# Performance work log

Measured on AMD Instinct MI355X. Metric: run time of the kernel, lower is better.

## Reference

```python
import jax, jax.numpy as jnp
import numpy as np

BIN_SIZE = 256
TOP_K = 16


def setup_inputs() -> dict:
    key = jax.random.key(0)
    kx, kc = jax.random.split(key)
    x = jax.random.normal(kx, (2, 4096, 512), dtype=jnp.float32)
    codebook = jax.random.normal(kc, (512, 16), dtype=jnp.float32)  # (feature_dim, max_num_bins//2)
    return {"x": x, "codebook": codebook}


def reference(x, codebook):
    B, N, F = x.shape
    n_bins = N // BIN_SIZE  # 16
    # LSH bucket assignment: project onto random hyperplanes, pick argmax of [p, -p]
    mul = x @ codebook[:, : n_bins // 2]                      # (B, N, n_bins//2)
    cmul = jnp.concatenate([mul, -mul], axis=-1)              # (B, N, n_bins)
    bin_idx = jnp.argmax(cmul, axis=-1)                       # (B, N)
    # argsort-based binning: equal-size bins of points sorted by bucket id
    bins_split = jnp.argsort(bin_idx, axis=-1).reshape(B, n_bins, BIN_SIZE)
    # gather points into bins: (B, n_bins, bin_size, F)
    points_binned = jnp.take_along_axis(x[:, None, :, :], bins_split[..., None], axis=2)
    # intra-bin dense similarity + sigmoid
    dm = jax.nn.sigmoid(jnp.einsum('bnif,bnjf->bnij', points_binned, points_binned))
    vals, idx = jax.lax.top_k(dm, TOP_K)                      # (B, n_bins, bin_size, k)
    # map local bin indices back to global point indices
    dst = jnp.take_along_axis(bins_split[:, :, None, :], idx, axis=-1)  # (B, nb, bs, k)
    src = jnp.broadcast_to(bins_split[..., None], dst.shape)
    b = jnp.broadcast_to(jnp.arange(B)[:, None, None, None], dst.shape)
    # dense equivalent of the coalesced batched sparse_coo_tensor of size (N, N)
    out = jnp.zeros((B, N, N), dtype=x.dtype).at[b, src, dst].add(vals)
    return out
```

## Files before the change

kernel.cpp:

```cpp
#include <hip/hip_runtime.h>
#include <stdint.h>
#include <math.h>

#define NPTS 4096
#define NF 512
#define NBINS 16
#define BSZ 256
#define TOPK 16
#define NBATCH 2
#define SHALF (NBATCH * NBINS * BSZ * BSZ)

__global__ __launch_bounds__(256) void k_assign(const float* __restrict__ x,
                                                const float* __restrict__ cb,
                                                int* __restrict__ bin_idx) {
    int gw   = (blockIdx.x * 256 + threadIdx.x) >> 6;
    int lane = threadIdx.x & 63;
    const float* row = x + (size_t)gw * NF;
    float acc[8];
#pragma unroll
    for (int j = 0; j < 8; j++) acc[j] = 0.f;
    for (int f = lane; f < NF; f += 64) {
        float xv = row[f];
        const float4* c = (const float4*)(cb + f * 16);
        float4 c0 = c[0], c1 = c[1];
        acc[0] += xv * c0.x; acc[1] += xv * c0.y; acc[2] += xv * c0.z; acc[3] += xv * c0.w;
        acc[4] += xv * c1.x; acc[5] += xv * c1.y; acc[6] += xv * c1.z; acc[7] += xv * c1.w;
    }
#pragma unroll
    for (int off = 32; off > 0; off >>= 1) {
#pragma unroll
        for (int j = 0; j < 8; j++) acc[j] += __shfl_xor(acc[j], off, 64);
    }
    if (lane == 0) {
        float best = acc[0]; int bi = 0;
#pragma unroll
        for (int j = 1; j < 8; j++) { if (acc[j] > best) { best = acc[j]; bi = j; } }
#pragma unroll
        for (int j = 0; j < 8; j++) { float v = -acc[j]; if (v > best) { best = v; bi = 8 + j; } }
        bin_idx[gw] = bi;
    }
}

__global__ __launch_bounds__(256) void k_sort(const int* __restrict__ bin_idx,
                                              int* __restrict__ order) {
    __shared__ int hist[NBINS][256];
    __shared__ int segsum[NBINS][16];
    __shared__ int segoff[NBINS][16];
    __shared__ int totals[NBINS];
    __shared__ int keybase[NBINS];
    int b = blockIdx.x, t = threadIdx.x;
    const int* bi = bin_idx + b * NPTS;
#pragma unroll
    for (int j = 0; j < NBINS; j++) hist[j][t] = 0;
    int base = t * 16;
    for (int i = 0; i < 16; i++) { int k = bi[base + i]; hist[k][t]++; }
    __syncthreads();
    {
        int j = t >> 4, sg = t & 15, s = 0;
#pragma unroll
        for (int u = 0; u < 16; u++) s += hist[j][sg * 16 + u];
        segsum[j][sg] = s;
    }
    __syncthreads();
    if (t < NBINS) {
        int run = 0;
#pragma unroll
        for (int sg = 0; sg < 16; sg++) { int c = segsum[t][sg]; segoff[t][sg] = run; run += c; }
        totals[t] = run;
    }
    __syncthreads();
    if (t == 0) {
        int run = 0;
#pragma unroll
        for (int j = 0; j < NBINS; j++) { keybase[j] = run; run += totals[j]; }
    }
    __syncthreads();
    {
        int j = t >> 4, sg = t & 15;
        int run = segoff[j][sg];
#pragma unroll
        for (int u = 0; u < 16; u++) { int c = hist[j][sg * 16 + u]; hist[j][sg * 16 + u] = run; run += c; }
    }
    __syncthreads();
    int* ob = order + b * NPTS;
    for (int i = 0; i < 16; i++) {
        int k = bi[base + i];
        int o = hist[k][t];
        hist[k][t] = o + 1;
        ob[keybase[k] + o] = base + i;
    }
}

__global__ __launch_bounds__(256) void k_gemm(const float* __restrict__ x,
                                              const int* __restrict__ order,
                                              float* __restrict__ S) {
    int blk = blockIdx.x;
    int kh  = blk & 1;
    int tn  = (blk >> 1) & 1;
    int tm  = (blk >> 2) & 1;
    int bin = (blk >> 3) & 15;
    int b   = blk >> 7;
    int t  = threadIdx.x;
    int tx = t & 15, ty = t >> 4;
    __shared__ int   idxA[128];
    __shared__ int   idxB[128];
    __shared__ float Asl[32][132];
    __shared__ float Bsl[32][132];
    int ob = b * NPTS + bin * BSZ;
    if (t < 128) idxA[t] = order[ob + tm * 128 + t];
    else         idxB[t - 128] = order[ob + tn * 128 + (t - 128)];
    __syncthreads();
    const float* xb = x + (size_t)b * (NPTS * NF);
    int rowi = t & 127;
    int qb   = t >> 7;
    const float* rowA = xb + (size_t)idxA[rowi] * NF + kh * 256;
    const float* rowB = xb + (size_t)idxB[rowi] * NF + kh * 256;
    float acc[8][8];
#pragma unroll
    for (int i = 0; i < 8; i++)
#pragma unroll
        for (int j = 0; j < 8; j++) acc[i][j] = 0.f;
    float4 pa[4], pb[4];
#pragma unroll
    for (int l = 0; l < 4; l++) {
        pa[l] = *(const float4*)(rowA + (qb + 2 * l) * 4);
        pb[l] = *(const float4*)(rowB + (qb + 2 * l) * 4);
    }
    for (int it = 0; it < 8; it++) {
        __syncthreads();
#pragma unroll
        for (int l = 0; l < 4; l++) {
            int kq = (qb + 2 * l) * 4;
            Asl[kq + 0][rowi] = pa[l].x; Asl[kq + 1][rowi] = pa[l].y;
            Asl[kq + 2][rowi] = pa[l].z; Asl[kq + 3][rowi] = pa[l].w;
            Bsl[kq + 0][rowi] = pb[l].x; Bsl[kq + 1][rowi] = pb[l].y;
            Bsl[kq + 2][rowi] = pb[l].z; Bsl[kq + 3][rowi] = pb[l].w;
        }
        __syncthreads();
        if (it < 7) {
            const float* a2 = rowA + (it + 1) * 32;
            const float* b2 = rowB + (it + 1) * 32;
#pragma unroll
            for (int l = 0; l < 4; l++) {
                pa[l] = *(const float4*)(a2 + (qb + 2 * l) * 4);
                pb[l] = *(const float4*)(b2 + (qb + 2 * l) * 4);
            }
        }
#pragma unroll
        for (int kk = 0; kk < 32; kk++) {
            float4 a0 = *(const float4*)&Asl[kk][ty * 8];
            float4 a1 = *(const float4*)&Asl[kk][ty * 8 + 4];
            float4 b0 = *(const float4*)&Bsl[kk][tx * 8];
            float4 b1 = *(const float4*)&Bsl[kk][tx * 8 + 4];
            float av[8] = {a0.x, a0.y, a0.z, a0.w, a1.x, a1.y, a1.z, a1.w};
            float bv[8] = {b0.x, b0.y, b0.z, b0.w, b1.x, b1.y, b1.z, b1.w};
#pragma unroll
            for (int i = 0; i < 8; i++)
#pragma unroll
                for (int j = 0; j < 8; j++) acc[i][j] += av[i] * bv[j];
        }
    }
    float* Sp = S + (size_t)kh * SHALF;
    size_t rowbase = (size_t)(b * NBINS + bin) * BSZ;
#pragma unroll
    for (int i = 0; i < 8; i++) {
        int r = tm * 128 + ty * 8 + i;
        float* orow = Sp + (rowbase + r) * BSZ + tn * 128 + tx * 8;
        *(float4*)(orow)     = make_float4(acc[i][0], acc[i][1], acc[i][2], acc[i][3]);
        *(float4*)(orow + 4) = make_float4(acc[i][4], acc[i][5], acc[i][6], acc[i][7]);
    }
}

__global__ __launch_bounds__(256) void k_topk(const float* __restrict__ S,
                                              const int* __restrict__ order,
                                              int* __restrict__ cols,
                                              float* __restrict__ vals) {
    int row  = (blockIdx.x * 256 + threadIdx.x) >> 6;
    int lane = threadIdx.x & 63;
    const float* s0 = S + (size_t)row * BSZ;
    const float* s1 = s0 + (size_t)SHALF;
    unsigned long long key[4];
#pragma unroll
    for (int q = 0; q < 4; q++) {
        int j = lane + 64 * q;
        float d = s0[j] + s1[j];
        float v = 1.0f / (1.0f + expf(-d));
        key[q] = ((unsigned long long)__float_as_uint(v) << 32) | (unsigned)(255 - j);
    }
    int myj = 0; float myv = 0.f;
#pragma unroll
    for (int it = 0; it < TOPK; it++) {
        unsigned long long k = key[0];
        if (key[1] > k) k = key[1];
        if (key[2] > k) k = key[2];
        if (key[3] > k) k = key[3];
#pragma unroll
        for (int off = 32; off > 0; off >>= 1) {
            unsigned long long o = __shfl_xor(k, off, 64);
            if (o > k) k = o;
        }
        int jw = 255 - (int)(k & 0xFFull);
        if (lane == it) { myj = jw; myv = __uint_as_float((unsigned)(k >> 32)); }
        if ((jw & 63) == lane) {
            int q = jw >> 6;
            if      (q == 0) key[0] = 0ull;
            else if (q == 1) key[1] = 0ull;
            else if (q == 2) key[2] = 0ull;
            else             key[3] = 0ull;
        }
    }
    if (lane < TOPK) {
        int b   = row >> 12;
        int bin = (row >> 8) & 15;
        int i   = row & 255;
        const int* obp = order + b * NPTS + bin * BSZ;
        int srcg = obp[i];
        int dstg = obp[myj];
        int o = (b * NPTS + srcg) * TOPK + lane;
        cols[o] = dstg;
        vals[o] = myv;
    }
}

__global__ __launch_bounds__(256) void k_write(const int* __restrict__ cols,
                                               const float* __restrict__ vals,
                                               float* __restrict__ out) {
    int row = blockIdx.x;
    int t   = threadIdx.x;
    float4* orow = (float4*)(out + (size_t)row * NPTS);
    float4 z = make_float4(0.f, 0.f, 0.f, 0.f);
#pragma unroll
    for (int u = 0; u < 4; u++) orow[t + 256 * u] = z;
    __syncthreads();
    if (t < TOPK) {
        int   c = cols[row * TOPK + t];
        float v = vals[row * TOPK + t];
        out[(size_t)row * NPTS + c] = v;
    }
}

extern "C" void kernel_launch(void* const* d_in, const int* in_sizes, int n_in,
                              void* d_out, int out_size, void* d_ws, size_t ws_size,
                              hipStream_t stream) {
    const float* x  = (const float*)d_in[0];
    const float* cb = (const float*)d_in[1];
    float* out = (float*)d_out;
    int*   bin_idx = (int*)d_ws;
    int*   order   = bin_idx + NBATCH * NPTS;
    int*   cols    = order + NBATCH * NPTS;
    float* vals    = (float*)(cols + NBATCH * NPTS * TOPK);
    float* S = out;

    k_assign<<<2048, 256, 0, stream>>>(x, cb, bin_idx);
    k_sort  <<<NBATCH, 256, 0, stream>>>(bin_idx, order);
    k_gemm  <<<256, 256, 0, stream>>>(x, order, S);
    k_topk  <<<2048, 256, 0, stream>>>(S, order, cols, vals);
    k_write <<<NBATCH * NPTS, 256, 0, stream>>>(cols, vals, out);
}
```

Baseline: 219.5 us.

## Split GEMM K dimension four ways and write output rows via LDS with nontemporal stores

The per-bin similarity GEMM now splits the 512-wide feature dimension into four partial sums instead of two. That doubles the block count to 512 so more CUs are busy, and launch bounds now ask for two blocks per CU. The top-k kernel sums four partial buffers held in the output scratch, so it reads more memory. The dense output writer now builds each row in shared memory, places the sparse values there, and streams the full row out with nontemporal vector stores. This avoids a separate scattered write after zeroing.

```diff
diff --git a/kernel.cpp b/kernel.cpp
--- a/kernel.cpp
+++ b/kernel.cpp
@@ -8,7 +8,10 @@
 #define BSZ 256
 #define TOPK 16
 #define NBATCH 2
-#define SHALF (NBATCH * NBINS * BSZ * BSZ)
+#define KSPLIT 4
+#define SPART (NBATCH * NBINS * BSZ * BSZ)
+
+typedef float vf4 __attribute__((ext_vector_type(4)));
 
 __global__ __launch_bounds__(256) void k_assign(const float* __restrict__ x,
                                                 const float* __restrict__ cb,
@@ -91,15 +94,15 @@
     }
 }
 
-__global__ __launch_bounds__(256) void k_gemm(const float* __restrict__ x,
-                                              const int* __restrict__ order,
-                                              float* __restrict__ S) {
+__global__ __launch_bounds__(256, 2) void k_gemm(const float* __restrict__ x,
+                                                 const int* __restrict__ order,
+                                                 float* __restrict__ S) {
     int blk = blockIdx.x;
-    int kh  = blk & 1;
-    int tn  = (blk >> 1) & 1;
-    int tm  = (blk >> 2) & 1;
-    int bin = (blk >> 3) & 15;
-    int b   = blk >> 7;
+    int kh  = blk & 3;
+    int tn  = (blk >> 2) & 1;
+    int tm  = (blk >> 3) & 1;
+    int bin = (blk >> 4) & 15;
+    int b   = blk >> 8;
     int t  = threadIdx.x;
     int tx = t & 15, ty = t >> 4;
     __shared__ int   idxA[128];
@@ -113,8 +116,8 @@
     const float* xb = x + (size_t)b * (NPTS * NF);
     int rowi = t & 127;
     int qb   = t >> 7;
-    const float* rowA = xb + (size_t)idxA[rowi] * NF + kh * 256;
-    const float* rowB = xb + (size_t)idxB[rowi] * NF + kh * 256;
+    const float* rowA = xb + (size_t)idxA[rowi] * NF + kh * 128;
+    const float* rowB = xb + (size_t)idxB[rowi] * NF + kh * 128;
     float acc[8][8];
 #pragma unroll
     for (int i = 0; i < 8; i++)
@@ -126,7 +129,7 @@
         pa[l] = *(const float4*)(rowA + (qb + 2 * l) * 4);
         pb[l] = *(const float4*)(rowB + (qb + 2 * l) * 4);
     }
-    for (int it = 0; it < 8; it++) {
+    for (int it = 0; it < 4; it++) {
         __syncthreads();
 #pragma unroll
         for (int l = 0; l < 4; l++) {
@@ -137,7 +140,7 @@
             Bsl[kq + 2][rowi] = pb[l].z; Bsl[kq + 3][rowi] = pb[l].w;
         }
         __syncthreads();
-        if (it < 7) {
+        if (it < 3) {
             const float* a2 = rowA + (it + 1) * 32;
             const float* b2 = rowB + (it + 1) * 32;
 #pragma unroll
@@ -160,7 +163,7 @@
                 for (int j = 0; j < 8; j++) acc[i][j] += av[i] * bv[j];
         }
     }
-    float* Sp = S + (size_t)kh * SHALF;
+    float* Sp = S + (size_t)kh * SPART;
     size_t rowbase = (size_t)(b * NBINS + bin) * BSZ;
 #pragma unroll
     for (int i = 0; i < 8; i++) {
@@ -178,12 +181,11 @@
     int row  = (blockIdx.x * 256 + threadIdx.x) >> 6;
     int lane = threadIdx.x & 63;
     const float* s0 = S + (size_t)row * BSZ;
-    const float* s1 = s0 + (size_t)SHALF;
     unsigned long long key[4];
 #pragma unroll
     for (int q = 0; q < 4; q++) {
         int j = lane + 64 * q;
-        float d = s0[j] + s1[j];
+        float d = s0[j] + s0[j + SPART] + s0[j + 2 * SPART] + s0[j + 3 * SPART];
         float v = 1.0f / (1.0f + expf(-d));
         key[q] = ((unsigned long long)__float_as_uint(v) << 32) | (unsigned)(255 - j);
     }
@@ -225,17 +227,22 @@
 __global__ __launch_bounds__(256) void k_write(const int* __restrict__ cols,
                                                const float* __restrict__ vals,
                                                float* __restrict__ out) {
+    __shared__ float buf[NPTS];
+    __shared__ int   pc[TOPK];
+    __shared__ float pv[TOPK];
     int row = blockIdx.x;
     int t   = threadIdx.x;
-    float4* orow = (float4*)(out + (size_t)row * NPTS);
-    float4 z = make_float4(0.f, 0.f, 0.f, 0.f);
-#pragma unroll
-    for (int u = 0; u < 4; u++) orow[t + 256 * u] = z;
-    __syncthreads();
-    if (t < TOPK) {
-        int   c = cols[row * TOPK + t];
-        float v = vals[row * TOPK + t];
-        out[(size_t)row * NPTS + c] = v;
+    if (t < TOPK) { pc[t] = cols[row * TOPK + t]; pv[t] = vals[row * TOPK + t]; }
+    vf4 z = {0.f, 0.f, 0.f, 0.f};
+#pragma unroll
+    for (int u = 0; u < 4; u++) ((vf4*)buf)[u * 256 + t] = z;
+    __syncthreads();
+    if (t < TOPK) buf[pc[t]] = pv[t];
+    __syncthreads();
+    vf4* orow = (vf4*)(out + (size_t)row * NPTS);
+#pragma unroll
+    for (int u = 0; u < 4; u++) {
+        __builtin_nontemporal_store(((const vf4*)buf)[u * 256 + t], &orow[u * 256 + t]);
     }
 }
 
@@ -253,7 +260,7 @@
 
     k_assign<<<2048, 256, 0, stream>>>(x, cb, bin_idx);
     k_sort  <<<NBATCH, 256, 0, stream>>>(bin_idx, order);
-    k_gemm  <<<256, 256, 0, stream>>>(x, order, S);
+    k_gemm  <<<512, 256, 0, stream>>>(x, order, S);
     k_topk  <<<2048, 256, 0, stream>>>(S, order, cols, vals);
     k_write <<<NBATCH * NPTS, 256, 0, stream>>>(cols, vals, out);
 }
```

Result: no change. 220.5 us (+0.5%).
